# Optimization experiments

Measured on AMD Instinct MI355X. Metric: run time of the kernel, lower is better.

## Reference

```python
import jax, jax.numpy as jnp
import numpy as np

B = 262144
NODE_ROWS, EDGE_ROWS, D = 19, 36, 4
KEEP = 4


def _make_sparse(key, rows):
    # each sample has exactly KEEP nonzero rows at random (sorted) positions
    k1, k2 = jax.random.split(key)
    perm = jnp.argsort(jax.random.uniform(k1, (B, rows)), axis=1)
    idx = jnp.sort(perm[:, :KEEP], axis=1)                      # (B, KEEP)
    vals = jax.random.normal(k2, (B, KEEP, D), dtype=jnp.float32) + 0.1
    x = jnp.zeros((B, rows, D), dtype=jnp.float32)
    x = x.at[jnp.arange(B)[:, None], idx].set(vals)
    return x.reshape(B, rows * D)


def setup_inputs() -> dict:
    key = jax.random.key(0)
    kn, ke, k1, k2, k3 = jax.random.split(key, 5)
    node = _make_sparse(kn, NODE_ROWS)   # (B, 76)
    edge = _make_sparse(ke, EDGE_ROWS)   # (B, 144)
    # MLP params (torch Linear default-ish init, stored as (in, out))
    def lin(k, fin, fout):
        ka, kb = jax.random.split(k)
        s = 1.0 / np.sqrt(fin)
        W = jax.random.uniform(ka, (fin, fout), jnp.float32, -s, s)
        b = jax.random.uniform(kb, (fout,), jnp.float32, -s, s)
        return W, b
    W1, b1 = lin(k1, 32, 256)
    W2, b2 = lin(k2, 256, 128)
    W3, b3 = lin(k3, 128, 34)
    return {"node": node, "edge": edge, "W1": W1, "b1": b1,
            "W2": W2, "b2": b2, "W3": W3, "b3": b3}


def _compact4(x):
    # x: (B, R, D) -> first 4 nonzero rows per sample, order preserved: (B, 4, D)
    mask = jnp.any(x != 0, axis=-1)                              # (B, R)
    idx = jnp.argsort(~mask, axis=1, stable=True)[:, :KEEP]      # (B, 4)
    return jnp.take_along_axis(x, idx[:, :, None], axis=1)


def reference(node, edge, W1, b1, W2, b2, W3, b3):
    n = _compact4(node.reshape(-1, NODE_ROWS, D))                # (B, 4, 4)
    e = _compact4(edge.reshape(-1, EDGE_ROWS, D))                # (B, 4, 4)
    x = jnp.concatenate([n, e], axis=-2).reshape(-1, 8 * D)      # (B, 32)
    x = jax.nn.relu(x @ W1 + b1)
    x = jax.nn.relu(x @ W2 + b2)
    x = x @ W3 + b3                                              # (B, 34)
    return jax.nn.log_softmax(x, axis=1)
```

## Files before the change

kernel.cpp:

```cpp
#include <hip/hip_runtime.h>
#include <stdint.h>
#include <stddef.h>

typedef __bf16 bf16;
typedef __attribute__((ext_vector_type(8))) __bf16 bf16x8;
typedef __attribute__((ext_vector_type(4))) __bf16 bf16x4;
typedef __attribute__((ext_vector_type(4))) float  f32x4;

#define W1OFF  0
#define W2OFF  (16*1024)
#define W3OFF  (80*1024)
#define BOFF   (92*1024)
#define IMGSZ  (92*1024 + 1728)
#define NCHUNK (IMGSZ/16)
#define PERW   3072
#define LDSSZ  (IMGSZ + 8*PERW)

#define SWZ(s) ((((s)>>1)&3)<<4)

__global__ void prep_kernel(const float* __restrict__ W1, const float* __restrict__ b1,
                            const float* __restrict__ W2, const float* __restrict__ b2,
                            const float* __restrict__ W3, const float* __restrict__ b3,
                            char* __restrict__ img)
{
  int tid = blockIdx.x * 256 + threadIdx.x;
  if (tid < 92 * 64) {
    int fid = tid >> 6, l = tid & 63;
    int m = l & 15, gg = l >> 4;
    const float* W; int stride, n, k0;
    if (fid < 16)      { W = W1; stride = 256; n = fid * 16 + m;            k0 = gg * 8; }
    else if (fid < 80) { int f = fid - 16; W = W2; stride = 128; n = (f >> 3) * 16 + m; k0 = (f & 7) * 32 + gg * 8; }
    else               { int f = fid - 80; W = W3; stride = 34;  n = (f >> 2) * 16 + m; k0 = (f & 3) * 32 + gg * 8; }
    bf16x8 v;
    #pragma unroll
    for (int j = 0; j < 8; ++j) {
      float x = (stride == 34 && n >= 34) ? 0.f : W[(size_t)(k0 + j) * stride + n];
      v[j] = (bf16)x;
    }
    *(bf16x8*)(img + (size_t)tid * 16) = v;
  } else if (tid < 92 * 64 + 432) {
    int i = tid - 92 * 64;
    float v;
    if (i < 256)      v = b1[i];
    else if (i < 384) v = b2[i - 256];
    else              { int j = i - 384; v = (j < 34) ? b3[j] : 0.f; }
    ((float*)(img + BOFF))[i] = v;
  }
}

__global__ __launch_bounds__(512, 2) void mlp_kernel(
    const float* __restrict__ node, const float* __restrict__ edge,
    const char* __restrict__ img, float* __restrict__ out)
{
  __shared__ __align__(16) char sm[LDSSZ];
  const int tid  = threadIdx.x;
  const int lane = tid & 63;
  const int w    = tid >> 6;
  const int blk  = blockIdx.x;

  for (int c = tid; c < NCHUNK; c += 512)
    *(f32x4*)(sm + (size_t)c * 16) = *(const f32x4*)(img + (size_t)c * 16);
  __syncthreads();

  char* const xb0 = sm + IMGSZ + w * PERW;
  char* const xb1 = xb0 + 1024;
  char* const stg = xb0 + 2048;
  const float* const b1p = (const float*)(sm + BOFF);
  const float* const b2p = b1p + 256;
  const float* const b3p = b1p + 384;

  const int g   = lane >> 4;
  const int m16 = lane & 15;
  const int cl  = lane & 3;
  const int sl  = lane >> 2;

  const float4* const np = (const float4*)node;
  const float4* const ep = (const float4*)edge;
  const f32x4 zf = {0.f, 0.f, 0.f, 0.f};

  float4 nf[5], ef[9];

  auto issue_loads = [&](int sbase) {
    const int s = sbase + sl;
    #pragma unroll
    for (int i = 0; i < 5; ++i) {
      const int r = cl + 4 * i;
      nf[i] = (r < 19) ? np[(size_t)s * 19 + r] : make_float4(0.f, 0.f, 0.f, 0.f);
    }
    #pragma unroll
    for (int i = 0; i < 9; ++i)
      ef[i] = ep[(size_t)s * 36 + cl + 4 * i];
  };

  auto compact = [&](char* dst) {
    uint32_t nm = 0; unsigned long long em = 0;
    #pragma unroll
    for (int i = 0; i < 5; ++i) {
      const int r = cl + 4 * i;
      if (r < 19 && (nf[i].x != 0.f || nf[i].y != 0.f || nf[i].z != 0.f || nf[i].w != 0.f))
        nm |= (1u << r);
    }
    #pragma unroll
    for (int i = 0; i < 9; ++i) {
      const int r = cl + 4 * i;
      if (ef[i].x != 0.f || ef[i].y != 0.f || ef[i].z != 0.f || ef[i].w != 0.f)
        em |= (1ull << r);
    }
    nm |= __shfl_xor(nm, 1); nm |= __shfl_xor(nm, 2);
    em |= __shfl_xor(em, 1); em |= __shfl_xor(em, 2);
    bf16x4 zb; zb[0] = (bf16)0.f; zb[1] = (bf16)0.f; zb[2] = (bf16)0.f; zb[3] = (bf16)0.f;
    *(bf16x4*)(dst + sl * 64 + ((8 * cl)      ^ SWZ(sl))) = zb;
    *(bf16x4*)(dst + sl * 64 + ((8 * cl + 32) ^ SWZ(sl))) = zb;
    #pragma unroll
    for (int i = 0; i < 5; ++i) {
      const int r = cl + 4 * i;
      if (r < 19 && ((nm >> r) & 1u)) {
        const int slot = __popc(nm & ((1u << r) - 1u));
        if (slot < 4) {
          bf16x4 pk; pk[0] = (bf16)nf[i].x; pk[1] = (bf16)nf[i].y; pk[2] = (bf16)nf[i].z; pk[3] = (bf16)nf[i].w;
          *(bf16x4*)(dst + sl * 64 + ((8 * slot) ^ SWZ(sl))) = pk;
        }
      }
    }
    #pragma unroll
    for (int i = 0; i < 9; ++i) {
      const int r = cl + 4 * i;
      if ((em >> r) & 1ull) {
        const int slot = __popcll(em & ((1ull << r) - 1ull));
        if (slot < 4) {
          bf16x4 pk; pk[0] = (bf16)ef[i].x; pk[1] = (bf16)ef[i].y; pk[2] = (bf16)ef[i].z; pk[3] = (bf16)ef[i].w;
          *(bf16x4*)(dst + sl * 64 + ((32 + 8 * slot) ^ SWZ(sl))) = pk;
        }
      }
    }
  };

  issue_loads(blk * 1024 + w * 16);
  compact(xb0);

  #pragma unroll 1
  for (int p = 0; p < 8; ++p) {
    char* const xb = (p & 1) ? xb1 : xb0;
    char* const xn = (p & 1) ? xb0 : xb1;
    const int S = blk * 1024 + p * 128 + w * 16;
    const bool pf = (p < 7);

    if (pf) issue_loads(S + 128);
    asm volatile("" ::: "memory");

    bf16x8 xf = *(const bf16x8*)(xb + m16 * 64 + ((16 * g) ^ SWZ(m16)));

    f32x4 acc2[8];
    #pragma unroll
    for (int i = 0; i < 8; ++i) acc2[i] = zf;

    #pragma unroll
    for (int kk = 0; kk < 8; ++kk) {
      #pragma unroll
      for (int t = 0; t < 2; ++t) {
        const int nt1 = kk * 2 + t;
        bf16x8 wf = *(const bf16x8*)(sm + W1OFF + nt1 * 1024 + lane * 16);
        f32x4 d = __builtin_amdgcn_mfma_f32_16x16x32_bf16(wf, xf, zf, 0, 0, 0);
        f32x4 b = *(const f32x4*)(b1p + nt1 * 16 + 4 * g);
        bf16x4 pk;
        #pragma unroll
        for (int r = 0; r < 4; ++r) pk[r] = (bf16)fmaxf(d[r] + b[r], 0.f);
        *(bf16x4*)(stg + m16 * 64 + ((32 * t + 8 * g) ^ SWZ(m16))) = pk;
      }
      bf16x8 sf = *(const bf16x8*)(stg + m16 * 64 + ((16 * g) ^ SWZ(m16)));
      #pragma unroll
      for (int nt2 = 0; nt2 < 8; ++nt2) {
        bf16x8 wf = *(const bf16x8*)(sm + W2OFF + (nt2 * 8 + kk) * 1024 + lane * 16);
        acc2[nt2] = __builtin_amdgcn_mfma_f32_16x16x32_bf16(wf, sf, acc2[nt2], 0, 0, 0);
      }
    }

    f32x4 acc3[3];
    #pragma unroll
    for (int i = 0; i < 3; ++i) acc3[i] = zf;

    #pragma unroll
    for (int k2 = 0; k2 < 4; ++k2) {
      #pragma unroll
      for (int t = 0; t < 2; ++t) {
        const int nt2 = k2 * 2 + t;
        f32x4 b = *(const f32x4*)(b2p + nt2 * 16 + 4 * g);
        bf16x4 pk;
        #pragma unroll
        for (int r = 0; r < 4; ++r) pk[r] = (bf16)fmaxf(acc2[nt2][r] + b[r], 0.f);
        *(bf16x4*)(stg + m16 * 64 + ((32 * t + 8 * g) ^ SWZ(m16))) = pk;
      }
      bf16x8 sf = *(const bf16x8*)(stg + m16 * 64 + ((16 * g) ^ SWZ(m16)));
      #pragma unroll
      for (int nt3 = 0; nt3 < 3; ++nt3) {
        bf16x8 wf = *(const bf16x8*)(sm + W3OFF + (nt3 * 4 + k2) * 1024 + lane * 16);
        acc3[nt3] = __builtin_amdgcn_mfma_f32_16x16x32_bf16(wf, sf, acc3[nt3], 0, 0, 0);
      }
    }

    float z[12];
    #pragma unroll
    for (int nt3 = 0; nt3 < 3; ++nt3) {
      f32x4 b = *(const f32x4*)(b3p + nt3 * 16 + 4 * g);
      #pragma unroll
      for (int r = 0; r < 4; ++r) {
        const int f = nt3 * 16 + 4 * g + r;
        z[nt3 * 4 + r] = (f < 34) ? (acc3[nt3][r] + b[r]) : -1e30f;
      }
    }
    float mx = z[0];
    #pragma unroll
    for (int i = 1; i < 12; ++i) mx = fmaxf(mx, z[i]);
    mx = fmaxf(mx, __shfl_xor(mx, 16));
    mx = fmaxf(mx, __shfl_xor(mx, 32));
    float sum = 0.f;
    #pragma unroll
    for (int i = 0; i < 12; ++i) sum += __expf(z[i] - mx);
    sum += __shfl_xor(sum, 16);
    sum += __shfl_xor(sum, 32);
    const float lse = mx + __logf(sum);

    float* orow = out + (size_t)(S + m16) * 34;
    *(float2*)(orow +  0 + 4 * g) = make_float2(z[0] - lse, z[1] - lse);
    *(float2*)(orow +  2 + 4 * g) = make_float2(z[2] - lse, z[3] - lse);
    *(float2*)(orow + 16 + 4 * g) = make_float2(z[4] - lse, z[5] - lse);
    *(float2*)(orow + 18 + 4 * g) = make_float2(z[6] - lse, z[7] - lse);
    if (g == 0)
      *(float2*)(orow + 32) = make_float2(z[8] - lse, z[9] - lse);

    if (pf) compact(xn);
  }
}

extern "C" void kernel_launch(void* const* d_in, const int* in_sizes, int n_in,
                              void* d_out, int out_size, void* d_ws, size_t ws_size,
                              hipStream_t stream)
{
  const float* node = (const float*)d_in[0];
  const float* edge = (const float*)d_in[1];
  const float* W1   = (const float*)d_in[2];
  const float* b1   = (const float*)d_in[3];
  const float* W2   = (const float*)d_in[4];
  const float* b2   = (const float*)d_in[5];
  const float* W3   = (const float*)d_in[6];
  const float* b3   = (const float*)d_in[7];
  char* img = (char*)d_ws;

  prep_kernel<<<25, 256, 0, stream>>>(W1, b1, W2, b2, W3, b3, img);
  mlp_kernel<<<256, 512, 0, stream>>>(node, edge, img, (float*)d_out);
}
```

Before: 62.10 us.

## Coalesce node/edge loads across wave and compact rows via ballot masks

```diff
diff --git a/kernel.cpp b/kernel.cpp
--- a/kernel.cpp
+++ b/kernel.cpp
@@ -3,6 +3,7 @@
 #include <stddef.h>
 
 typedef __bf16 bf16;
+typedef unsigned long long u64;
 typedef __attribute__((ext_vector_type(8))) __bf16 bf16x8;
 typedef __attribute__((ext_vector_type(4))) __bf16 bf16x4;
 typedef __attribute__((ext_vector_type(4))) float  f32x4;
@@ -48,6 +49,8 @@
   }
 }
 
+#define NZ4(v) ((v).x != 0.f || (v).y != 0.f || (v).z != 0.f || (v).w != 0.f)
+
 __global__ __launch_bounds__(512, 2) void mlp_kernel(
     const float* __restrict__ node, const float* __restrict__ edge,
     const char* __restrict__ img, float* __restrict__ out)
@@ -81,57 +84,95 @@
   float4 nf[5], ef[9];
 
   auto issue_loads = [&](int sbase) {
-    const int s = sbase + sl;
-    #pragma unroll
-    for (int i = 0; i < 5; ++i) {
-      const int r = cl + 4 * i;
-      nf[i] = (r < 19) ? np[(size_t)s * 19 + r] : make_float4(0.f, 0.f, 0.f, 0.f);
-    }
-    #pragma unroll
-    for (int i = 0; i < 9; ++i)
-      ef[i] = ep[(size_t)s * 36 + cl + 4 * i];
+    const float4* bn = np + (size_t)sbase * 19;
+    const float4* be = ep + (size_t)sbase * 36;
+    #pragma unroll
+    for (int j = 0; j < 5; ++j) {
+      int idx = j * 64 + lane;
+      if (j == 4) idx = idx < 304 ? idx : 303;
+      nf[j] = bn[idx];
+    }
+    #pragma unroll
+    for (int j = 0; j < 9; ++j)
+      ef[j] = be[j * 64 + lane];
   };
 
   auto compact = [&](char* dst) {
-    uint32_t nm = 0; unsigned long long em = 0;
-    #pragma unroll
-    for (int i = 0; i < 5; ++i) {
-      const int r = cl + 4 * i;
-      if (r < 19 && (nf[i].x != 0.f || nf[i].y != 0.f || nf[i].z != 0.f || nf[i].w != 0.f))
-        nm |= (1u << r);
-    }
-    #pragma unroll
-    for (int i = 0; i < 9; ++i) {
-      const int r = cl + 4 * i;
-      if (ef[i].x != 0.f || ef[i].y != 0.f || ef[i].z != 0.f || ef[i].w != 0.f)
-        em |= (1ull << r);
-    }
-    nm |= __shfl_xor(nm, 1); nm |= __shfl_xor(nm, 2);
-    em |= __shfl_xor(em, 1); em |= __shfl_xor(em, 2);
     bf16x4 zb; zb[0] = (bf16)0.f; zb[1] = (bf16)0.f; zb[2] = (bf16)0.f; zb[3] = (bf16)0.f;
     *(bf16x4*)(dst + sl * 64 + ((8 * cl)      ^ SWZ(sl))) = zb;
     *(bf16x4*)(dst + sl * 64 + ((8 * cl + 32) ^ SWZ(sl))) = zb;
-    #pragma unroll
-    for (int i = 0; i < 5; ++i) {
-      const int r = cl + 4 * i;
-      if (r < 19 && ((nm >> r) & 1u)) {
-        const int slot = __popc(nm & ((1u << r) - 1u));
+
+    auto node_row = [&](int j, u64 bm1, u64 b, u64 bp1, const float4& v) {
+      int idx = j * 64 + lane;
+      if (j == 4) idx = idx < 304 ? idx : 303;
+      int s = idx / 19, r = idx % 19;
+      int pos = idx - r;
+      int word = pos >> 6, sh = pos & 63;
+      bool wj = (word == j);
+      u64 lo = wj ? b : bm1;
+      u64 hi = wj ? bp1 : b;
+      u64 m = lo >> sh;
+      if (sh) m |= hi << (64 - sh);
+      unsigned int m19 = (unsigned int)m & 0x7FFFFu;
+      if ((m19 >> r) & 1u) {
+        int slot = __popc(m19 & ((1u << r) - 1u));
         if (slot < 4) {
-          bf16x4 pk; pk[0] = (bf16)nf[i].x; pk[1] = (bf16)nf[i].y; pk[2] = (bf16)nf[i].z; pk[3] = (bf16)nf[i].w;
-          *(bf16x4*)(dst + sl * 64 + ((8 * slot) ^ SWZ(sl))) = pk;
+          bf16x4 pk; pk[0] = (bf16)v.x; pk[1] = (bf16)v.y; pk[2] = (bf16)v.z; pk[3] = (bf16)v.w;
+          *(bf16x4*)(dst + s * 64 + ((8 * slot) ^ SWZ(s))) = pk;
         }
       }
-    }
-    #pragma unroll
-    for (int i = 0; i < 9; ++i) {
-      const int r = cl + 4 * i;
-      if ((em >> r) & 1ull) {
-        const int slot = __popcll(em & ((1ull << r) - 1ull));
+    };
+    auto edge_row = [&](int j, u64 bm1, u64 b, u64 bp1, const float4& v) {
+      int idx = j * 64 + lane;
+      int s = idx / 36, r = idx % 36;
+      int pos = idx - r;
+      int word = pos >> 6, sh = pos & 63;
+      bool wj = (word == j);
+      u64 lo = wj ? b : bm1;
+      u64 hi = wj ? bp1 : b;
+      u64 m = lo >> sh;
+      if (sh) m |= hi << (64 - sh);
+      m &= 0xFFFFFFFFFull;
+      if ((m >> r) & 1ull) {
+        int slot = __popcll(m & ((1ull << r) - 1ull));
         if (slot < 4) {
-          bf16x4 pk; pk[0] = (bf16)ef[i].x; pk[1] = (bf16)ef[i].y; pk[2] = (bf16)ef[i].z; pk[3] = (bf16)ef[i].w;
-          *(bf16x4*)(dst + sl * 64 + ((32 + 8 * slot) ^ SWZ(sl))) = pk;
+          bf16x4 pk; pk[0] = (bf16)v.x; pk[1] = (bf16)v.y; pk[2] = (bf16)v.z; pk[3] = (bf16)v.w;
+          *(bf16x4*)(dst + s * 64 + ((32 + 8 * slot) ^ SWZ(s))) = pk;
         }
       }
+    };
+
+    {
+      u64 n0 = __ballot(NZ4(nf[0]));
+      u64 n1 = __ballot(NZ4(nf[1]));
+      u64 n2 = __ballot(NZ4(nf[2]));
+      u64 n3 = __ballot(NZ4(nf[3]));
+      u64 n4 = __ballot(NZ4(nf[4]));
+      node_row(0, 0,  n0, n1, nf[0]);
+      node_row(1, n0, n1, n2, nf[1]);
+      node_row(2, n1, n2, n3, nf[2]);
+      node_row(3, n2, n3, n4, nf[3]);
+      node_row(4, n3, n4, 0,  nf[4]);
+    }
+    {
+      u64 e0 = __ballot(NZ4(ef[0]));
+      u64 e1 = __ballot(NZ4(ef[1]));
+      u64 e2 = __ballot(NZ4(ef[2]));
+      u64 e3 = __ballot(NZ4(ef[3]));
+      u64 e4 = __ballot(NZ4(ef[4]));
+      u64 e5 = __ballot(NZ4(ef[5]));
+      u64 e6 = __ballot(NZ4(ef[6]));
+      u64 e7 = __ballot(NZ4(ef[7]));
+      u64 e8 = __ballot(NZ4(ef[8]));
+      edge_row(0, 0,  e0, e1, ef[0]);
+      edge_row(1, e0, e1, e2, ef[1]);
+      edge_row(2, e1, e2, e3, ef[2]);
+      edge_row(3, e2, e3, e4, ef[3]);
+      edge_row(4, e3, e4, e5, ef[4]);
+      edge_row(5, e4, e5, e6, ef[5]);
+      edge_row(6, e5, e6, e7, ef[6]);
+      edge_row(7, e6, e7, e8, ef[7]);
+      edge_row(8, e7, e8, 0,  ef[8]);
     }
   };
 
```

Measured after the change: 70.52 us. 13.6% more time.
